# Kernel tuning notes

Hardware: AMD Instinct MI355X
Metric: run time of the kernel (lower is better)

The kernel has to match this reference:

```python
import jax, jax.numpy as jnp
import numpy as np

N_NODES = 100000
N_EDGES = 1600000
F_IN = 512
HEADS = 8
C1 = 8            # hidden per head in conv1
N_CLASSES = 40
NEG_SLOPE = 0.2
EPS = 1e-16


def setup_inputs() -> dict:
    key = jax.random.key(0)
    ks = jax.random.split(key, 12)
    x = jax.random.normal(ks[0], (N_NODES, F_IN), dtype=jnp.float32)
    # edges with src != dst (PyG SuperGAT removes then re-adds self-loops)
    src = jax.random.randint(ks[1], (N_EDGES,), 0, N_NODES)
    off = jax.random.randint(ks[2], (N_EDGES,), 1, N_NODES)
    dst = (src + off) % N_NODES
    edge_index = jnp.stack([src, dst]).astype(jnp.int64)
    def glorot(k, shape):
        fan = shape[0] + shape[-1]
        return jax.random.uniform(k, shape, jnp.float32, -1.0, 1.0) * np.sqrt(6.0 / fan)
    W1 = glorot(ks[3], (F_IN, HEADS * C1))
    att_l1 = glorot(ks[4], (HEADS, C1))
    att_r1 = glorot(ks[5], (HEADS, C1))
    b1 = jnp.zeros((HEADS * C1,), jnp.float32)
    W2 = glorot(ks[6], (HEADS * C1, HEADS * N_CLASSES))
    att_l2 = glorot(ks[7], (HEADS, N_CLASSES))
    att_r2 = glorot(ks[8], (HEADS, N_CLASSES))
    b2 = jnp.zeros((N_CLASSES,), jnp.float32)
    return {"x": x, "edge_index": edge_index, "W1": W1, "att_l1": att_l1,
            "att_r1": att_r1, "b1": b1, "W2": W2, "att_l2": att_l2,
            "att_r2": att_r2, "b2": b2}


def supergat_conv(x, edge_index, W, att_l, att_r, bias, concat):
    """SuperGATConv with attention_type='MX', eval mode (no dropout)."""
    N = x.shape[0]
    H, C = att_l.shape
    xw = (x @ W).reshape(N, H, C)
    loops = jnp.arange(N)
    src = jnp.concatenate([edge_index[0], loops])  # j (source)
    dst = jnp.concatenate([edge_index[1], loops])  # i (target)
    x_j = xw[src]                                   # [E,H,C]
    x_i = xw[dst]                                   # [E,H,C]
    # MX attention: GO score gated by sigmoid of DP logits
    logits = jnp.einsum('ehc,ehc->eh', x_i, x_j)
    alpha = jnp.einsum('ehc,hc->eh', x_j, att_l) + jnp.einsum('ehc,hc->eh', x_i, att_r)
    alpha = alpha * jax.nn.sigmoid(logits)
    alpha = jax.nn.leaky_relu(alpha, NEG_SLOPE)
    # segment softmax over incoming edges of each destination node
    amax = jax.ops.segment_max(alpha, dst, num_segments=N)
    e = jnp.exp(alpha - amax[dst])
    denom = jax.ops.segment_sum(e, dst, num_segments=N)
    a = e / (denom[dst] + EPS)
    out = jax.ops.segment_sum(x_j * a[..., None], dst, num_segments=N)  # [N,H,C]
    out = out.reshape(N, H * C) if concat else out.mean(axis=1)
    return out + bias


def reference(x, edge_index, W1, att_l1, att_r1, b1, W2, att_l2, att_r2, b2):
    # eval mode: F.dropout(p=0.6) is identity, att_loss is 0
    h = jax.nn.elu(supergat_conv(x, edge_index, W1, att_l1, att_r1, b1, concat=True))
    out = supergat_conv(h, edge_index, W2, att_l2, att_r2, b2, concat=False)
    att_loss = jnp.float32(0.0)
    return jax.nn.log_softmax(out, axis=-1), att_loss
```

## Files before the change

### kernel.cpp

```cpp
#include <hip/hip_runtime.h>
#include <cstdint>

#define N_NODES 100000
#define N_EDGES 1600000
#define SCAN_NB 196

typedef short bf16x8 __attribute__((ext_vector_type(8)));
typedef float f32x4 __attribute__((ext_vector_type(4)));
typedef float f32x2 __attribute__((ext_vector_type(2)));

__device__ __forceinline__ uint16_t f2bf(float f) {
    uint32_t b = __float_as_uint(f);
    return (uint16_t)((b + 0x7fffu + ((b >> 16) & 1u)) >> 16);
}
__device__ __forceinline__ float bfval(uint16_t u) {
    return __uint_as_float(((uint32_t)u) << 16);
}
__device__ __forceinline__ float blo(uint32_t u) { return __uint_as_float(u << 16); }
__device__ __forceinline__ float bhi(uint32_t u) { return __uint_as_float(u & 0xffff0000u); }

__device__ __forceinline__ float fast_rcp(float x) { return __builtin_amdgcn_rcpf(x); }
__device__ __forceinline__ float dpp_xadd1(float x) {
    int s = __builtin_amdgcn_update_dpp(0, __float_as_int(x), 0xB1, 0xF, 0xF, true);
    return x + __int_as_float(s);
}
__device__ __forceinline__ float dpp_xadd2(float x) {
    int s = __builtin_amdgcn_update_dpp(0, __float_as_int(x), 0x4E, 0xF, 0xF, true);
    return x + __int_as_float(s);
}

__global__ void cvt_w1(const float* __restrict__ W1, uint16_t* __restrict__ whi,
                       uint16_t* __restrict__ wlo) {
    int gid = blockIdx.x * 256 + threadIdx.x;
    int c = gid & 63, kg = gid >> 6;
    uint32_t dh[4], dl[4];
    #pragma unroll
    for (int t = 0; t < 4; ++t) {
        float v0 = W1[(kg * 8 + 2 * t) * 64 + c];
        float v1 = W1[(kg * 8 + 2 * t + 1) * 64 + c];
        uint16_t h0 = f2bf(v0), h1 = f2bf(v1);
        uint16_t l0 = f2bf(v0 - bfval(h0)), l1 = f2bf(v1 - bfval(h1));
        dh[t] = h0 | ((uint32_t)h1 << 16);
        dl[t] = l0 | ((uint32_t)l1 << 16);
    }
    *(uint4*)(whi + (long)c * 512 + kg * 8) = make_uint4(dh[0], dh[1], dh[2], dh[3]);
    *(uint4*)(wlo + (long)c * 512 + kg * 8) = make_uint4(dl[0], dl[1], dl[2], dl[3]);
}

__global__ void cvt_w2(const float* __restrict__ W2, uint16_t* __restrict__ w2T) {
    int c = blockIdx.x * 64 + threadIdx.x;
    if (c >= 320) return;
    for (int kg = 0; kg < 8; ++kg) {
        uint32_t d[4];
        #pragma unroll
        for (int t = 0; t < 4; ++t) {
            float v0 = W2[(kg * 8 + 2 * t) * 320 + c];
            float v1 = W2[(kg * 8 + 2 * t + 1) * 320 + c];
            d[t] = f2bf(v0) | ((uint32_t)f2bf(v1) << 16);
        }
        *(uint4*)(w2T + (long)c * 64 + kg * 8) = make_uint4(d[0], d[1], d[2], d[3]);
    }
}

__global__ __launch_bounds__(256) void wvec_k(const float* __restrict__ W2,
        const float* __restrict__ attl, const float* __restrict__ attr,
        float* __restrict__ wl2, float* __restrict__ wr2) {
    int t = blockIdx.x * 256 + threadIdx.x;
    if (t >= 512) return;
    int h = t >> 6, k = t & 63;
    float sl = 0.f, sr = 0.f;
    #pragma unroll 8
    for (int c = 0; c < 40; ++c) {
        float w = W2[k * 320 + h * 40 + c];
        sl += w * attl[h * 40 + c];
        sr += w * attr[h * 40 + c];
    }
    wl2[t] = sl; wr2[t] = sr;
}

__global__ __launch_bounds__(512) void gemm1_mfma(const float* __restrict__ x,
        const uint16_t* __restrict__ w1hi, const uint16_t* __restrict__ w1lo,
        float* __restrict__ xw1) {
    __shared__ __align__(16) char Ah[128 * 144];
    __shared__ __align__(16) char Al[128 * 144];
    __shared__ __align__(16) char Bh[64 * 144];
    __shared__ __align__(16) char Bl[64 * 144];
    int tid = threadIdx.x;
    int l = tid & 63, w = tid >> 6;
    long base = (long)blockIdx.x * 128;
    f32x4 acc[4];
    #pragma unroll
    for (int ct = 0; ct < 4; ++ct)
        #pragma unroll
        for (int j = 0; j < 4; ++j) acc[ct][j] = 0.f;

    for (int kb = 0; kb < 512; kb += 64) {
        __syncthreads();
        #pragma unroll
        for (int it = 0; it < 2; ++it) {
            int idx = tid + it * 512;
            int row = idx >> 3, kc = idx & 7;
            long r = base + row; if (r >= N_NODES) r = N_NODES - 1;
            const float4* p = (const float4*)(x + r * 512 + kb + kc * 8);
            float4 f0 = p[0], f1 = p[1];
            float v[8] = {f0.x, f0.y, f0.z, f0.w, f1.x, f1.y, f1.z, f1.w};
            uint32_t dh[4], dl[4];
            #pragma unroll
            for (int t = 0; t < 4; ++t) {
                uint16_t h0 = f2bf(v[2 * t]),     h1 = f2bf(v[2 * t + 1]);
                uint16_t l0 = f2bf(v[2 * t] - bfval(h0));
                uint16_t l1 = f2bf(v[2 * t + 1] - bfval(h1));
                dh[t] = h0 | ((uint32_t)h1 << 16);
                dl[t] = l0 | ((uint32_t)l1 << 16);
            }
            *(uint4*)(Ah + row * 144 + kc * 16) = make_uint4(dh[0], dh[1], dh[2], dh[3]);
            *(uint4*)(Al + row * 144 + kc * 16) = make_uint4(dl[0], dl[1], dl[2], dl[3]);
        }
        {
            int c = tid >> 3, kc = tid & 7;
            *(uint4*)(Bh + c * 144 + kc * 16) =
                *(const uint4*)(w1hi + (long)c * 512 + kb + kc * 8);
            *(uint4*)(Bl + c * 144 + kc * 16) =
                *(const uint4*)(w1lo + (long)c * 512 + kb + kc * 8);
        }
        __syncthreads();
        #pragma unroll
        for (int kk = 0; kk < 2; ++kk) {
            int aoff = (w * 16 + (l & 15)) * 144 + kk * 64 + (l >> 4) * 16;
            bf16x8 ah = *(const bf16x8*)(Ah + aoff);
            bf16x8 alo = *(const bf16x8*)(Al + aoff);
            #pragma unroll
            for (int ct = 0; ct < 4; ++ct) {
                int boff = (ct * 16 + (l & 15)) * 144 + kk * 64 + (l >> 4) * 16;
                bf16x8 bh = *(const bf16x8*)(Bh + boff);
                bf16x8 bl = *(const bf16x8*)(Bl + boff);
                acc[ct] = __builtin_amdgcn_mfma_f32_16x16x32_bf16(ah, bh, acc[ct], 0, 0, 0);
                acc[ct] = __builtin_amdgcn_mfma_f32_16x16x32_bf16(alo, bh, acc[ct], 0, 0, 0);
                acc[ct] = __builtin_amdgcn_mfma_f32_16x16x32_bf16(ah, bl, acc[ct], 0, 0, 0);
            }
        }
    }
    int nrow = w * 16 + (l >> 4) * 4;
    #pragma unroll
    for (int ct = 0; ct < 4; ++ct)
        #pragma unroll
        for (int j = 0; j < 4; ++j) {
            long node = base + nrow + j;
            if (node < N_NODES) xw1[node * 64 + ct * 16 + (l & 15)] = acc[ct][j];
        }
}

__global__ __launch_bounds__(512) void gemm2_mfma(const float* __restrict__ h,
        const uint16_t* __restrict__ w2T, uint16_t* __restrict__ xw2) {
    __shared__ __align__(16) char Bsm[320 * 144];
    int tid = threadIdx.x;
    int l = tid & 63, w = tid >> 6;
    long base = (long)blockIdx.x * 128;
    #pragma unroll
    for (int it = 0; it < 5; ++it) {
        int idx = tid + it * 512;
        int c = idx >> 3, kc = idx & 7;
        *(uint4*)(Bsm + c * 144 + kc * 16) = *(const uint4*)(w2T + (long)c * 64 + kc * 8);
    }
    long n0 = base + w * 16 + (l & 15);
    long nld = n0 < N_NODES ? n0 : N_NODES - 1;
    bf16x8 ah[2], alo[2];
    #pragma unroll
    for (int kk = 0; kk < 2; ++kk) {
        const float4* p = (const float4*)(h + nld * 64 + kk * 32 + (l >> 4) * 8);
        float4 f0 = p[0], f1 = p[1];
        float v[8] = {f0.x, f0.y, f0.z, f0.w, f1.x, f1.y, f1.z, f1.w};
        bf16x8 hv, lv;
        #pragma unroll
        for (int t = 0; t < 8; ++t) {
            uint16_t hh = f2bf(v[t]);
            hv[t] = (short)hh;
            lv[t] = (short)f2bf(v[t] - bfval(hh));
        }
        ah[kk] = hv; alo[kk] = lv;
    }
    __syncthreads();
    f32x4 acc[20];
    #pragma unroll
    for (int ct = 0; ct < 20; ++ct)
        #pragma unroll
        for (int j = 0; j < 4; ++j) acc[ct][j] = 0.f;
    #pragma unroll
    for (int ct = 0; ct < 20; ++ct) {
        #pragma unroll
        for (int kk = 0; kk < 2; ++kk) {
            bf16x8 b = *(const bf16x8*)(Bsm + (ct * 16 + (l & 15)) * 144 + kk * 64 + (l >> 4) * 16);
            acc[ct] = __builtin_amdgcn_mfma_f32_16x16x32_bf16(b, ah[kk], acc[ct], 0, 0, 0);
            acc[ct] = __builtin_amdgcn_mfma_f32_16x16x32_bf16(b, alo[kk], acc[ct], 0, 0, 0);
        }
    }
    if (n0 < N_NODES) {
        #pragma unroll
        for (int ct = 0; ct < 20; ++ct) {
            uint32_t d0 = f2bf(acc[ct][0]) | ((uint32_t)f2bf(acc[ct][1]) << 16);
            uint32_t d1 = f2bf(acc[ct][2]) | ((uint32_t)f2bf(acc[ct][3]) << 16);
            int cb = ct * 16 + (l >> 4) * 4;
            *(uint32_t*)(xw2 + n0 * 320 + cb) = d0;
            *(uint32_t*)(xw2 + n0 * 320 + cb + 2) = d1;
        }
    }
}

__global__ void hist_k(const int* __restrict__ dst, int* __restrict__ deg) {
    int e = blockIdx.x * blockDim.x + threadIdx.x;
    if (e < N_EDGES) atomicAdd(&deg[dst[e]], 1);
}

__global__ __launch_bounds__(512) void scan_a(const int* __restrict__ deg,
        int* __restrict__ offs, int* __restrict__ btot) {
    __shared__ int sh[512];
    int t = threadIdx.x;
    int g = blockIdx.x * 512 + t;
    int v = (g < N_NODES) ? deg[g] : 0;
    sh[t] = v;
    __syncthreads();
    #pragma unroll
    for (int o = 1; o < 512; o <<= 1) {
        int add = (t >= o) ? sh[t - o] : 0;
        __syncthreads();
        sh[t] += add;
        __syncthreads();
    }
    if (g < N_NODES) offs[g] = sh[t] - v;
    if (t == 511) btot[blockIdx.x] = sh[511];
}

__global__ __launch_bounds__(256) void scan_b(int* __restrict__ btot) {
    __shared__ int sh[256];
    int t = threadIdx.x;
    int v = (t < SCAN_NB) ? btot[t] : 0;
    sh[t] = v;
    __syncthreads();
    #pragma unroll
    for (int o = 1; o < 256; o <<= 1) {
        int add = (t >= o) ? sh[t - o] : 0;
        __syncthreads();
        sh[t] += add;
        __syncthreads();
    }
    if (t < SCAN_NB) btot[t] = sh[t] - v;
}

__global__ __launch_bounds__(512) void scan_c(int* __restrict__ offs,
        const int* __restrict__ btot, int* __restrict__ cursor) {
    int g = blockIdx.x * 512 + threadIdx.x;
    if (g < N_NODES) {
        int o = offs[g] + btot[blockIdx.x];
        offs[g] = o;
        cursor[g] = o;
    }
}

__global__ void scatter_k(const int* __restrict__ src, const int* __restrict__ dst,
        int* __restrict__ cursor, int* __restrict__ csr8) {
    int e = blockIdx.x * blockDim.x + threadIdx.x;
    if (e < N_EDGES) {
        int pos = atomicAdd(&cursor[dst[e]], 1);
        csr8[pos] = src[e] << 3;
    }
}

__global__ __launch_bounds__(256) void conv1_node(const float* __restrict__ xw,
        const int* __restrict__ offs, const int* __restrict__ deg,
        const int* __restrict__ csr8, const float* __restrict__ att_l,
        const float* __restrict__ att_r, const float* __restrict__ b1,
        float* __restrict__ hout) {
    int wid = (blockIdx.x * blockDim.x + threadIdx.x) >> 6;
    if (wid >= N_NODES) return;
    int i = wid;
    int lane = threadIdx.x & 63;
    int g = lane >> 3, h = lane & 7;
    const float4* rowi = (const float4*)(xw + (long)i * 64 + h * 8);
    float4 xi0 = rowi[0], xi1 = rowi[1];
    f32x2 xip[4] = {{xi0.x, xi0.y}, {xi0.z, xi0.w}, {xi1.x, xi1.y}, {xi1.z, xi1.w}};
    const float4* alp4 = (const float4*)(att_l + h * 8);
    float4 t0 = alp4[0], t1 = alp4[1];
    f32x2 atlp[4] = {{t0.x, t0.y}, {t0.z, t0.w}, {t1.x, t1.y}, {t1.z, t1.w}};
    const float4* arp4 = (const float4*)(att_r + h * 8);
    float4 u0 = arp4[0], u1 = arp4[1];
    f32x2 atrp[4] = {{u0.x, u0.y}, {u0.z, u0.w}, {u1.x, u1.y}, {u1.z, u1.w}};
    f32x2 prp = xip[0] * atrp[0];
    prp += xip[1] * atrp[1];
    prp += xip[2] * atrp[2];
    prp += xip[3] * atrp[3];
    float pr = prp.x + prp.y;
    f32x2 accp[4] = {{0.f,0.f},{0.f,0.f},{0.f,0.f},{0.f,0.f}};
    float den = 0.f;

#define C1_EDGE(XJP) do { \
    f32x2 qdp = xip[0] * (XJP)[0]; \
    qdp += xip[1] * (XJP)[1]; \
    qdp += xip[2] * (XJP)[2]; \
    qdp += xip[3] * (XJP)[3]; \
    f32x2 qlp = (XJP)[0] * atlp[0]; \
    qlp += (XJP)[1] * atlp[1]; \
    qlp += (XJP)[2] * atlp[2]; \
    qlp += (XJP)[3] * atlp[3]; \
    float qd = qdp.x + qdp.y, ql = qlp.x + qlp.y; \
    float a = (ql + pr) * fast_rcp(1.0f + __expf(-qd)); \
    a = fmaxf(a, 0.2f * a); \
    float e = __expf(a); \
    den += e; \
    f32x2 ev = {e, e}; \
    accp[0] += ev * (XJP)[0]; \
    accp[1] += ev * (XJP)[1]; \
    accp[2] += ev * (XJP)[2]; \
    accp[3] += ev * (XJP)[3]; \
} while (0)

    if (g == 0) C1_EDGE(xip);
    int off = offs[i], dg = deg[i];
    int k = g;
    for (; k + 8 < dg; k += 16) {
        int j0 = csr8[off + k], j1 = csr8[off + k + 8];
        const float4* r0 = (const float4*)(xw + (long)j0 * 8 + h * 8);
        const float4* r1 = (const float4*)(xw + (long)j1 * 8 + h * 8);
        float4 a0 = r0[0], a1 = r0[1];
        float4 b0 = r1[0], b1v = r1[1];
        f32x2 ap[4] = {{a0.x, a0.y}, {a0.z, a0.w}, {a1.x, a1.y}, {a1.z, a1.w}};
        f32x2 bp[4] = {{b0.x, b0.y}, {b0.z, b0.w}, {b1v.x, b1v.y}, {b1v.z, b1v.w}};
        C1_EDGE(ap);
        C1_EDGE(bp);
    }
    if (k < dg) {
        int j0 = csr8[off + k];
        const float4* r0 = (const float4*)(xw + (long)j0 * 8 + h * 8);
        float4 a0 = r0[0], a1 = r0[1];
        f32x2 ap[4] = {{a0.x, a0.y}, {a0.z, a0.w}, {a1.x, a1.y}, {a1.z, a1.w}};
        C1_EDGE(ap);
    }
#undef C1_EDGE

    float acc[8] = {accp[0].x, accp[0].y, accp[1].x, accp[1].y,
                    accp[2].x, accp[2].y, accp[3].x, accp[3].y};
    #pragma unroll
    for (int o = 8; o <= 32; o <<= 1) {
        #pragma unroll
        for (int t = 0; t < 8; ++t) acc[t] += __shfl_xor(acc[t], o);
        den += __shfl_xor(den, o);
    }
    if (g == 0) {
        float inv = fast_rcp(den + 1e-16f);
        const float4* bp4 = (const float4*)(b1 + h * 8);
        float4 c0 = bp4[0], c1 = bp4[1];
        float4 o0, o1;
        float v;
        v = acc[0]*inv + c0.x; o0.x = v > 0.f ? v : __expf(v) - 1.0f;
        v = acc[1]*inv + c0.y; o0.y = v > 0.f ? v : __expf(v) - 1.0f;
        v = acc[2]*inv + c0.z; o0.z = v > 0.f ? v : __expf(v) - 1.0f;
        v = acc[3]*inv + c0.w; o0.w = v > 0.f ? v : __expf(v) - 1.0f;
        v = acc[4]*inv + c1.x; o1.x = v > 0.f ? v : __expf(v) - 1.0f;
        v = acc[5]*inv + c1.y; o1.y = v > 0.f ? v : __expf(v) - 1.0f;
        v = acc[6]*inv + c1.z; o1.z = v > 0.f ? v : __expf(v) - 1.0f;
        v = acc[7]*inv + c1.w; o1.w = v > 0.f ? v : __expf(v) - 1.0f;
        float4* po = (float4*)(hout + (long)i * 64 + h * 8);
        po[0] = o0; po[1] = o1;
    }
}

__global__ __launch_bounds__(256) void node_att2h(const float* __restrict__ hbuf,
        const float* __restrict__ wl2, const float* __restrict__ wr2,
        float* __restrict__ al, float* __restrict__ ar) {
    __shared__ float lw[512], lr[512];
    int tid = threadIdx.x;
    for (int t = tid; t < 512; t += 256) { lw[t] = wl2[t]; lr[t] = wr2[t]; }
    __syncthreads();
    int i = blockIdx.x * 256 + tid;
    if (i >= N_NODES) return;
    const float4* row = (const float4*)(hbuf + (long)i * 64);
    float sl[8] = {0,0,0,0,0,0,0,0}, sr[8] = {0,0,0,0,0,0,0,0};
    #pragma unroll
    for (int d4 = 0; d4 < 16; ++d4) {
        float4 v = row[d4];
        #pragma unroll
        for (int hh = 0; hh < 8; ++hh) {
            const float4 wv = *(const float4*)(lw + hh * 64 + d4 * 4);
            const float4 rv = *(const float4*)(lr + hh * 64 + d4 * 4);
            sl[hh] += v.x*wv.x + v.y*wv.y + v.z*wv.z + v.w*wv.w;
            sr[hh] += v.x*rv.x + v.y*rv.y + v.z*rv.z + v.w*rv.w;
        }
    }
    #pragma unroll
    for (int hh = 0; hh < 8; ++hh) {
        al[i * 8 + hh] = sl[hh];
        ar[i * 8 + hh] = sr[hh];
    }
}

__device__ __forceinline__ int fidx(const int* __restrict__ csr8, int pos, int valid) {
    int p = pos < N_EDGES ? pos : N_EDGES - 1;
    int j = csr8[p];
    return valid ? j : 0;
}

__global__ __launch_bounds__(256) void conv2_node(const uint16_t* __restrict__ xw,
        const int* __restrict__ offs, const int* __restrict__ deg,
        const int* __restrict__ csr8, const float* __restrict__ al,
        const float* __restrict__ ar, const float* __restrict__ b2,
        float* __restrict__ out) {
    if (blockIdx.x == 0 && threadIdx.x == 0) out[(long)N_NODES * 40] = 0.0f;
    int wid = (blockIdx.x * blockDim.x + threadIdx.x) >> 6;
    if (wid >= N_NODES) return;
    int i = wid;
    int lane = threadIdx.x & 63;
    int half = lane >> 5, l = lane & 31;
    int h = l >> 2, q = l & 3;
    const uint32_t* xwd = (const uint32_t*)xw;
    unsigned lq4 = 20u * (unsigned)h + 4u * (unsigned)q;
    unsigned lq1 = 20u * (unsigned)h + 16u + (unsigned)q;

    f32x2 xip[5];
    {
        const uint32_t* rowi = xwd + (unsigned)i * 160u;
        uint4 qi = *(const uint4*)(rowi + lq4);
        uint32_t ti = rowi[lq1];
        xip[0] = (f32x2){blo(qi.x), bhi(qi.x)};
        xip[1] = (f32x2){blo(qi.y), bhi(qi.y)};
        xip[2] = (f32x2){blo(qi.z), bhi(qi.z)};
        xip[3] = (f32x2){blo(qi.w), bhi(qi.w)};
        xip[4] = (f32x2){blo(ti),   bhi(ti)};
    }
    float ari = ar[i * 8 + h];
    f32x2 accp[5] = {{0.f,0.f},{0.f,0.f},{0.f,0.f},{0.f,0.f},{0.f,0.f}};
    float den = 0.f;

#define C2_CORE(ALJ, XJP) do { \
    f32x2 pdp = xip[0] * (XJP)[0]; \
    pdp += xip[1] * (XJP)[1]; \
    pdp += xip[2] * (XJP)[2]; \
    pdp += xip[3] * (XJP)[3]; \
    pdp += xip[4] * (XJP)[4]; \
    float pd = pdp.x + pdp.y; \
    pd = dpp_xadd1(pd); \
    pd = dpp_xadd2(pd); \
    float a = ((ALJ) + ari) * fast_rcp(1.0f + __expf(-pd)); \
    a = fmaxf(a, 0.2f * a); \
    float e = __expf(a); \
    den += e; \
    f32x2 ev = {e, e}; \
    accp[0] += ev * (XJP)[0]; \
    accp[1] += ev * (XJP)[1]; \
    accp[2] += ev * (XJP)[2]; \
    accp[3] += ev * (XJP)[3]; \
    accp[4] += ev * (XJP)[4]; \
} while (0)

#define C2_UNPACK(DST, U) do { \
    _Pragma("unroll") \
    for (int t = 0; t < 5; ++t) (DST)[t] = (f32x2){blo((U)[t]), bhi((U)[t])}; \
} while (0)

#define C2_FETCH(J, BUF, ALV) do { \
    const uint32_t* _r = xwd + (unsigned)(J) * 20u; \
    uint4 _q = *(const uint4*)(_r + lq4); \
    (BUF)[0] = _q.x; (BUF)[1] = _q.y; (BUF)[2] = _q.z; (BUF)[3] = _q.w; \
    (BUF)[4] = _r[lq1]; \
    (ALV) = al[(J) + h]; \
} while (0)

    if (half == 0) C2_CORE(al[i * 8 + h], xip);
    int off = offs[i], dg = deg[i];

    int k = half;
    int v0 = (k < dg), v1 = (k + 2 < dg);
    int j0 = fidx(csr8, off + k, v0);
    int j1 = fidx(csr8, off + k + 2, v1);
    uint32_t cA[5], cB[5], dA[5], dB[5];
    float alA, alB, alC, alD;
    C2_FETCH(j0, cA, alA);
    C2_FETCH(j1, cB, alB);
    while (v0) {
        int k4 = k + 4;
        int w0 = (k4 < dg), w1 = (k4 + 2 < dg);
        int m0 = fidx(csr8, off + k4, w0);
        int m1 = fidx(csr8, off + k4 + 2, w1);
        C2_FETCH(m0, dA, alC);
        C2_FETCH(m1, dB, alD);
        { f32x2 xj[5]; C2_UNPACK(xj, cA); C2_CORE(alA, xj); }
        if (v1) { f32x2 xj[5]; C2_UNPACK(xj, cB); C2_CORE(alB, xj); }
        if (!w0) break;
        int k8 = k + 8;
        v0 = (k8 < dg); v1 = (k8 + 2 < dg);
        int p0 = fidx(csr8, off + k8, v0);
        int p1 = fidx(csr8, off + k8 + 2, v1);
        C2_FETCH(p0, cA, alA);
        C2_FETCH(p1, cB, alB);
        { f32x2 xj[5]; C2_UNPACK(xj, dA); C2_CORE(alC, xj); }
        if (w1) { f32x2 xj[5]; C2_UNPACK(xj, dB); C2_CORE(alD, xj); }
        k = k8;
    }
#undef C2_CORE
#undef C2_UNPACK
#undef C2_FETCH

    float acc[10] = {accp[0].x, accp[0].y, accp[1].x, accp[1].y, accp[2].x,
                     accp[2].y, accp[3].x, accp[3].y, accp[4].x, accp[4].y};
    #pragma unroll
    for (int t = 0; t < 10; ++t) acc[t] += __shfl_xor(acc[t], 32);
    den += __shfl_xor(den, 32);
    float inv = 0.125f * fast_rcp(den + 1e-16f);
    #pragma unroll
    for (int t = 0; t < 10; ++t) acc[t] *= inv;
    #pragma unroll
    for (int o = 4; o <= 16; o <<= 1) {
        #pragma unroll
        for (int t = 0; t < 10; ++t) acc[t] += __shfl_xor(acc[t], o);
    }
    #pragma unroll
    for (int t = 0; t < 8; ++t) acc[t] += b2[8 * q + t];
    acc[8] += b2[32 + 2 * q];
    acc[9] += b2[33 + 2 * q];
    float mx = acc[0];
    #pragma unroll
    for (int t = 1; t < 10; ++t) mx = fmaxf(mx, acc[t]);
    mx = fmaxf(mx, __shfl_xor(mx, 1));
    mx = fmaxf(mx, __shfl_xor(mx, 2));
    float s = 0.f;
    #pragma unroll
    for (int t = 0; t < 10; ++t) s += __expf(acc[t] - mx);
    s += __shfl_xor(s, 1);
    s += __shfl_xor(s, 2);
    float lse = mx + __logf(s);
    if (lane < 4) {
        float4* po = (float4*)(out + (long)i * 40 + 8 * q);
        po[0] = make_float4(acc[0] - lse, acc[1] - lse, acc[2] - lse, acc[3] - lse);
        po[1] = make_float4(acc[4] - lse, acc[5] - lse, acc[6] - lse, acc[7] - lse);
        float2* pt = (float2*)(out + (long)i * 40 + 32 + 2 * q);
        *pt = make_float2(acc[8] - lse, acc[9] - lse);
    }
}

extern "C" void kernel_launch(void* const* d_in, const int* in_sizes, int n_in,
                              void* d_out, int out_size, void* d_ws, size_t ws_size,
                              hipStream_t stream) {
    const float* x      = (const float*)d_in[0];
    const int*   ei     = (const int*)d_in[1];
    const float* W1     = (const float*)d_in[2];
    const float* att_l1 = (const float*)d_in[3];
    const float* att_r1 = (const float*)d_in[4];
    const float* b1     = (const float*)d_in[5];
    const float* W2     = (const float*)d_in[6];
    const float* att_l2 = (const float*)d_in[7];
    const float* att_r2 = (const float*)d_in[8];
    const float* b2     = (const float*)d_in[9];
    const int* src = ei;
    const int* dst = ei + N_EDGES;
    float* out = (float*)d_out;

    char* ws = (char*)d_ws;
    float*    xw1    = (float*)(ws + 0);
    float*    hbuf   = (float*)(ws + 25600000);
    uint16_t* xw2b   = (uint16_t*)(ws + 51200000);
    float*    al     = (float*)(ws + 115200000);
    float*    ar     = (float*)(ws + 118400000);
    int*      deg    = (int*)(ws + 121600000);
    int*      offs   = (int*)(ws + 122000000);
    int*      cursor = (int*)(ws + 122400000);
    int*      btot   = (int*)(ws + 122800000);
    int*      csr8   = (int*)(ws + 122801024);
    uint16_t* w1hi   = (uint16_t*)(ws + 129201024);
    uint16_t* w1lo   = (uint16_t*)(ws + 129266560);
    uint16_t* w2T    = (uint16_t*)(ws + 129332096);
    float*    wl2    = (float*)(ws + 129373056);
    float*    wr2    = (float*)(ws + 129375104);

    hipMemsetAsync(deg, 0, (size_t)N_NODES * 4, stream);

    cvt_w1<<<16, 256, 0, stream>>>(W1, w1hi, w1lo);
    cvt_w2<<<5, 64, 0, stream>>>(W2, w2T);
    wvec_k<<<2, 256, 0, stream>>>(W2, att_l2, att_r2, wl2, wr2);

    hist_k<<<6250, 256, 0, stream>>>(dst, deg);
    scan_a<<<SCAN_NB, 512, 0, stream>>>(deg, offs, btot);
    scan_b<<<1, 256, 0, stream>>>(btot);
    scan_c<<<SCAN_NB, 512, 0, stream>>>(offs, btot, cursor);
    scatter_k<<<6250, 256, 0, stream>>>(src, dst, cursor, csr8);

    gemm1_mfma<<<782, 512, 0, stream>>>(x, w1hi, w1lo, xw1);
    conv1_node<<<25000, 256, 0, stream>>>(xw1, offs, deg, csr8, att_l1, att_r1, b1, hbuf);
    node_att2h<<<391, 256, 0, stream>>>(hbuf, wl2, wr2, al, ar);

    gemm2_mfma<<<782, 512, 0, stream>>>(hbuf, w2T, xw2b);
    conv2_node<<<25000, 256, 0, stream>>>(xw2b, offs, deg, csr8, al, ar, b2, out);
}
```

Before: 538.0 us.

## Fuse weight prep kernels, gather bf16 neighbor rows, fold attention projections into conv1

Merges the three small weight-conversion kernels into one launch. gemm1 now also writes a bf16 copy of xw1, and conv1 gathers neighbor rows from that copy, halving the bytes moved per edge gather. The per-node conv2 attention projections (al/ar) are computed inside conv1 from the ELU output, removing the separate node_att2h pass over hbuf. The cost is reduced precision on gathered source features and an extra bf16 store in gemm1. The bf16 buffer aliases xw2b, which is safe only because xw2b is written after conv1 finishes.

```diff
diff --git a/kernel.cpp b/kernel.cpp
--- a/kernel.cpp
+++ b/kernel.cpp
@@ -29,58 +29,58 @@
     return x + __int_as_float(s);
 }
 
-__global__ void cvt_w1(const float* __restrict__ W1, uint16_t* __restrict__ whi,
-                       uint16_t* __restrict__ wlo) {
-    int gid = blockIdx.x * 256 + threadIdx.x;
-    int c = gid & 63, kg = gid >> 6;
-    uint32_t dh[4], dl[4];
-    #pragma unroll
-    for (int t = 0; t < 4; ++t) {
-        float v0 = W1[(kg * 8 + 2 * t) * 64 + c];
-        float v1 = W1[(kg * 8 + 2 * t + 1) * 64 + c];
-        uint16_t h0 = f2bf(v0), h1 = f2bf(v1);
-        uint16_t l0 = f2bf(v0 - bfval(h0)), l1 = f2bf(v1 - bfval(h1));
-        dh[t] = h0 | ((uint32_t)h1 << 16);
-        dl[t] = l0 | ((uint32_t)l1 << 16);
-    }
-    *(uint4*)(whi + (long)c * 512 + kg * 8) = make_uint4(dh[0], dh[1], dh[2], dh[3]);
-    *(uint4*)(wlo + (long)c * 512 + kg * 8) = make_uint4(dl[0], dl[1], dl[2], dl[3]);
-}
-
-__global__ void cvt_w2(const float* __restrict__ W2, uint16_t* __restrict__ w2T) {
-    int c = blockIdx.x * 64 + threadIdx.x;
-    if (c >= 320) return;
-    for (int kg = 0; kg < 8; ++kg) {
-        uint32_t d[4];
+__global__ __launch_bounds__(512) void prep_k(const float* __restrict__ W1,
+        const float* __restrict__ W2, const float* __restrict__ attl,
+        const float* __restrict__ attr,
+        uint16_t* __restrict__ w1hi, uint16_t* __restrict__ w1lo,
+        float* __restrict__ wl2, float* __restrict__ wr2,
+        uint16_t* __restrict__ w2T) {
+    int b = blockIdx.x, tid = threadIdx.x;
+    if (b < 8) {
+        int gid = b * 512 + tid;
+        int c = gid & 63, kg = gid >> 6;
+        uint32_t dh[4], dl[4];
         #pragma unroll
         for (int t = 0; t < 4; ++t) {
-            float v0 = W2[(kg * 8 + 2 * t) * 320 + c];
-            float v1 = W2[(kg * 8 + 2 * t + 1) * 320 + c];
-            d[t] = f2bf(v0) | ((uint32_t)f2bf(v1) << 16);
-        }
-        *(uint4*)(w2T + (long)c * 64 + kg * 8) = make_uint4(d[0], d[1], d[2], d[3]);
-    }
-}
-
-__global__ __launch_bounds__(256) void wvec_k(const float* __restrict__ W2,
-        const float* __restrict__ attl, const float* __restrict__ attr,
-        float* __restrict__ wl2, float* __restrict__ wr2) {
-    int t = blockIdx.x * 256 + threadIdx.x;
-    if (t >= 512) return;
-    int h = t >> 6, k = t & 63;
-    float sl = 0.f, sr = 0.f;
-    #pragma unroll 8
-    for (int c = 0; c < 40; ++c) {
-        float w = W2[k * 320 + h * 40 + c];
-        sl += w * attl[h * 40 + c];
-        sr += w * attr[h * 40 + c];
-    }
-    wl2[t] = sl; wr2[t] = sr;
+            float v0 = W1[(kg * 8 + 2 * t) * 64 + c];
+            float v1 = W1[(kg * 8 + 2 * t + 1) * 64 + c];
+            uint16_t h0 = f2bf(v0), h1 = f2bf(v1);
+            uint16_t l0 = f2bf(v0 - bfval(h0)), l1 = f2bf(v1 - bfval(h1));
+            dh[t] = h0 | ((uint32_t)h1 << 16);
+            dl[t] = l0 | ((uint32_t)l1 << 16);
+        }
+        *(uint4*)(w1hi + (long)c * 512 + kg * 8) = make_uint4(dh[0], dh[1], dh[2], dh[3]);
+        *(uint4*)(w1lo + (long)c * 512 + kg * 8) = make_uint4(dl[0], dl[1], dl[2], dl[3]);
+    } else if (b == 8) {
+        int h = tid >> 6, k = tid & 63;
+        float sl = 0.f, sr = 0.f;
+        #pragma unroll 8
+        for (int c = 0; c < 40; ++c) {
+            float w = W2[k * 320 + h * 40 + c];
+            sl += w * attl[h * 40 + c];
+            sr += w * attr[h * 40 + c];
+        }
+        wl2[tid] = sl; wr2[tid] = sr;
+    } else {
+        int c = tid;
+        if (c < 320) {
+            for (int kg = 0; kg < 8; ++kg) {
+                uint32_t d[4];
+                #pragma unroll
+                for (int t = 0; t < 4; ++t) {
+                    float v0 = W2[(kg * 8 + 2 * t) * 320 + c];
+                    float v1 = W2[(kg * 8 + 2 * t + 1) * 320 + c];
+                    d[t] = f2bf(v0) | ((uint32_t)f2bf(v1) << 16);
+                }
+                *(uint4*)(w2T + (long)c * 64 + kg * 8) = make_uint4(d[0], d[1], d[2], d[3]);
+            }
+        }
+    }
 }
 
 __global__ __launch_bounds__(512) void gemm1_mfma(const float* __restrict__ x,
         const uint16_t* __restrict__ w1hi, const uint16_t* __restrict__ w1lo,
-        float* __restrict__ xw1) {
+        float* __restrict__ xw1, uint16_t* __restrict__ xw1b) {
     __shared__ __align__(16) char Ah[128 * 144];
     __shared__ __align__(16) char Al[128 * 144];
     __shared__ __align__(16) char Bh[64 * 144];
@@ -146,7 +146,11 @@
         #pragma unroll
         for (int j = 0; j < 4; ++j) {
             long node = base + nrow + j;
-            if (node < N_NODES) xw1[node * 64 + ct * 16 + (l & 15)] = acc[ct][j];
+            if (node < N_NODES) {
+                int col = ct * 16 + (l & 15);
+                xw1[node * 64 + col] = acc[ct][j];
+                xw1b[node * 64 + col] = f2bf(acc[ct][j]);
+            }
         }
 }
 
@@ -266,10 +270,12 @@
 }
 
 __global__ __launch_bounds__(256) void conv1_node(const float* __restrict__ xw,
+        const uint16_t* __restrict__ xwb,
         const int* __restrict__ offs, const int* __restrict__ deg,
         const int* __restrict__ csr8, const float* __restrict__ att_l,
         const float* __restrict__ att_r, const float* __restrict__ b1,
-        float* __restrict__ hout) {
+        const float* __restrict__ wl2, const float* __restrict__ wr2,
+        float* __restrict__ hout, float* __restrict__ al, float* __restrict__ ar) {
     int wid = (blockIdx.x * blockDim.x + threadIdx.x) >> 6;
     if (wid >= N_NODES) return;
     int i = wid;
@@ -318,20 +324,20 @@
     int k = g;
     for (; k + 8 < dg; k += 16) {
         int j0 = csr8[off + k], j1 = csr8[off + k + 8];
-        const float4* r0 = (const float4*)(xw + (long)j0 * 8 + h * 8);
-        const float4* r1 = (const float4*)(xw + (long)j1 * 8 + h * 8);
-        float4 a0 = r0[0], a1 = r0[1];
-        float4 b0 = r1[0], b1v = r1[1];
-        f32x2 ap[4] = {{a0.x, a0.y}, {a0.z, a0.w}, {a1.x, a1.y}, {a1.z, a1.w}};
-        f32x2 bp[4] = {{b0.x, b0.y}, {b0.z, b0.w}, {b1v.x, b1v.y}, {b1v.z, b1v.w}};
+        uint4 q0 = *(const uint4*)(xwb + (long)j0 * 8 + h * 8);
+        uint4 q1 = *(const uint4*)(xwb + (long)j1 * 8 + h * 8);
+        f32x2 ap[4] = {{blo(q0.x), bhi(q0.x)}, {blo(q0.y), bhi(q0.y)},
+                       {blo(q0.z), bhi(q0.z)}, {blo(q0.w), bhi(q0.w)}};
+        f32x2 bp[4] = {{blo(q1.x), bhi(q1.x)}, {blo(q1.y), bhi(q1.y)},
+                       {blo(q1.z), bhi(q1.z)}, {blo(q1.w), bhi(q1.w)}};
         C1_EDGE(ap);
         C1_EDGE(bp);
     }
     if (k < dg) {
         int j0 = csr8[off + k];
-        const float4* r0 = (const float4*)(xw + (long)j0 * 8 + h * 8);
-        float4 a0 = r0[0], a1 = r0[1];
-        f32x2 ap[4] = {{a0.x, a0.y}, {a0.z, a0.w}, {a1.x, a1.y}, {a1.z, a1.w}};
+        uint4 q0 = *(const uint4*)(xwb + (long)j0 * 8 + h * 8);
+        f32x2 ap[4] = {{blo(q0.x), bhi(q0.x)}, {blo(q0.y), bhi(q0.y)},
+                       {blo(q0.z), bhi(q0.z)}, {blo(q0.w), bhi(q0.w)}};
         C1_EDGE(ap);
     }
 #undef C1_EDGE
@@ -344,51 +350,39 @@
         for (int t = 0; t < 8; ++t) acc[t] += __shfl_xor(acc[t], o);
         den += __shfl_xor(den, o);
     }
+    float inv = fast_rcp(den + 1e-16f);
+    const float4* bp4 = (const float4*)(b1 + h * 8);
+    float4 c0 = bp4[0], c1 = bp4[1];
+    float bias[8] = {c0.x, c0.y, c0.z, c0.w, c1.x, c1.y, c1.z, c1.w};
+    float ov[8];
+    #pragma unroll
+    for (int t = 0; t < 8; ++t) {
+        float v = acc[t] * inv + bias[t];
+        ov[t] = v > 0.f ? v : __expf(v) - 1.0f;
+    }
     if (g == 0) {
-        float inv = fast_rcp(den + 1e-16f);
-        const float4* bp4 = (const float4*)(b1 + h * 8);
-        float4 c0 = bp4[0], c1 = bp4[1];
-        float4 o0, o1;
-        float v;
-        v = acc[0]*inv + c0.x; o0.x = v > 0.f ? v : __expf(v) - 1.0f;
-        v = acc[1]*inv + c0.y; o0.y = v > 0.f ? v : __expf(v) - 1.0f;
-        v = acc[2]*inv + c0.z; o0.z = v > 0.f ? v : __expf(v) - 1.0f;
-        v = acc[3]*inv + c0.w; o0.w = v > 0.f ? v : __expf(v) - 1.0f;
-        v = acc[4]*inv + c1.x; o1.x = v > 0.f ? v : __expf(v) - 1.0f;
-        v = acc[5]*inv + c1.y; o1.y = v > 0.f ? v : __expf(v) - 1.0f;
-        v = acc[6]*inv + c1.z; o1.z = v > 0.f ? v : __expf(v) - 1.0f;
-        v = acc[7]*inv + c1.w; o1.w = v > 0.f ? v : __expf(v) - 1.0f;
         float4* po = (float4*)(hout + (long)i * 64 + h * 8);
-        po[0] = o0; po[1] = o1;
-    }
-}
-
-__global__ __launch_bounds__(256) void node_att2h(const float* __restrict__ hbuf,
-        const float* __restrict__ wl2, const float* __restrict__ wr2,
-        float* __restrict__ al, float* __restrict__ ar) {
-    __shared__ float lw[512], lr[512];
-    int tid = threadIdx.x;
-    for (int t = tid; t < 512; t += 256) { lw[t] = wl2[t]; lr[t] = wr2[t]; }
-    __syncthreads();
-    int i = blockIdx.x * 256 + tid;
-    if (i >= N_NODES) return;
-    const float4* row = (const float4*)(hbuf + (long)i * 64);
-    float sl[8] = {0,0,0,0,0,0,0,0}, sr[8] = {0,0,0,0,0,0,0,0};
-    #pragma unroll
-    for (int d4 = 0; d4 < 16; ++d4) {
-        float4 v = row[d4];
-        #pragma unroll
-        for (int hh = 0; hh < 8; ++hh) {
-            const float4 wv = *(const float4*)(lw + hh * 64 + d4 * 4);
-            const float4 rv = *(const float4*)(lr + hh * 64 + d4 * 4);
-            sl[hh] += v.x*wv.x + v.y*wv.y + v.z*wv.z + v.w*wv.w;
-            sr[hh] += v.x*rv.x + v.y*rv.y + v.z*rv.z + v.w*rv.w;
-        }
-    }
-    #pragma unroll
-    for (int hh = 0; hh < 8; ++hh) {
-        al[i * 8 + hh] = sl[hh];
-        ar[i * 8 + hh] = sr[hh];
+        po[0] = make_float4(ov[0], ov[1], ov[2], ov[3]);
+        po[1] = make_float4(ov[4], ov[5], ov[6], ov[7]);
+    }
+    {
+        const float4* wlp = (const float4*)(wl2 + g * 64 + h * 8);
+        float4 w0 = wlp[0], w1 = wlp[1];
+        const float4* wrp = (const float4*)(wr2 + g * 64 + h * 8);
+        float4 r0 = wrp[0], r1 = wrp[1];
+        float sl = ov[0]*w0.x + ov[1]*w0.y + ov[2]*w0.z + ov[3]*w0.w
+                 + ov[4]*w1.x + ov[5]*w1.y + ov[6]*w1.z + ov[7]*w1.w;
+        float sr = ov[0]*r0.x + ov[1]*r0.y + ov[2]*r0.z + ov[3]*r0.w
+                 + ov[4]*r1.x + ov[5]*r1.y + ov[6]*r1.z + ov[7]*r1.w;
+        #pragma unroll
+        for (int o = 1; o <= 4; o <<= 1) {
+            sl += __shfl_xor(sl, o);
+            sr += __shfl_xor(sr, o);
+        }
+        if (h == 0) {
+            al[i * 8 + g] = sl;
+            ar[i * 8 + g] = sr;
+        }
     }
 }
 
@@ -556,6 +550,7 @@
     float*    xw1    = (float*)(ws + 0);
     float*    hbuf   = (float*)(ws + 25600000);
     uint16_t* xw2b   = (uint16_t*)(ws + 51200000);
+    uint16_t* xw1b   = (uint16_t*)(ws + 51200000);
     float*    al     = (float*)(ws + 115200000);
     float*    ar     = (float*)(ws + 118400000);
     int*      deg    = (int*)(ws + 121600000);
@@ -571,9 +566,8 @@
 
     hipMemsetAsync(deg, 0, (size_t)N_NODES * 4, stream);
 
-    cvt_w1<<<16, 256, 0, stream>>>(W1, w1hi, w1lo);
-    cvt_w2<<<5, 64, 0, stream>>>(W2, w2T);
-    wvec_k<<<2, 256, 0, stream>>>(W2, att_l2, att_r2, wl2, wr2);
+    prep_k<<<10, 512, 0, stream>>>(W1, W2, att_l2, att_r2,
+                                   w1hi, w1lo, wl2, wr2, w2T);
 
     hist_k<<<6250, 256, 0, stream>>>(dst, deg);
     scan_a<<<SCAN_NB, 512, 0, stream>>>(deg, offs, btot);
@@ -581,9 +575,10 @@
     scan_c<<<SCAN_NB, 512, 0, stream>>>(offs, btot, cursor);
     scatter_k<<<6250, 256, 0, stream>>>(src, dst, cursor, csr8);
 
-    gemm1_mfma<<<782, 512, 0, stream>>>(x, w1hi, w1lo, xw1);
-    conv1_node<<<25000, 256, 0, stream>>>(xw1, offs, deg, csr8, att_l1, att_r1, b1, hbuf);
-    node_att2h<<<391, 256, 0, stream>>>(hbuf, wl2, wr2, al, ar);
+    gemm1_mfma<<<782, 512, 0, stream>>>(x, w1hi, w1lo, xw1, xw1b);
+    conv1_node<<<25000, 256, 0, stream>>>(xw1, xw1b, offs, deg, csr8,
+                                          att_l1, att_r1, b1, wl2, wr2,
+                                          hbuf, al, ar);
 
     gemm2_mfma<<<782, 512, 0, stream>>>(hbuf, w2T, xw2b);
     conv2_node<<<25000, 256, 0, stream>>>(xw2b, offs, deg, csr8, al, ar, b2, out);
```

After: 526.9 us. -2.1%, faster.
